# Optimization experiments

Hardware: AMD Instinct MI355X
Metric: run time of the kernel (lower is better)

The kernel has to match this reference:

```python
import jax, jax.numpy as jnp
import numpy as np

N_NODES = 50000
N_EDGES = 800000
HIDDEN = 128
MLP_DIM = 64

def setup_inputs() -> dict:
    key = jax.random.key(0)
    k1, k2, k3, k4 = jax.random.split(key, 4)
    node_emb = jax.random.normal(k1, (N_NODES, HIDDEN), dtype=jnp.float32)
    edge_index = jax.random.randint(k2, (2, N_EDGES), 0, N_NODES, dtype=jnp.int64)
    # Xavier-uniform init like the torch module
    lim1 = float(np.sqrt(6.0 / (2 * HIDDEN + MLP_DIM)))
    lim2 = float(np.sqrt(6.0 / (MLP_DIM + 1)))
    W1 = jax.random.uniform(k3, (2 * HIDDEN, MLP_DIM), minval=-lim1, maxval=lim1, dtype=jnp.float32)
    b1 = jnp.zeros((MLP_DIM,), dtype=jnp.float32)
    W2 = jax.random.uniform(k4, (MLP_DIM, 1), minval=-lim2, maxval=lim2, dtype=jnp.float32)
    b2 = jnp.zeros((1,), dtype=jnp.float32)
    return {"node_emb": node_emb, "edge_index": edge_index, "W1": W1, "b1": b1, "W2": W2, "b2": b2}

def reference(node_emb, edge_index, W1, b1, W2, b2):
    src, dst = edge_index[0], edge_index[1]
    emb_src = node_emb[src]                      # [E, H] gather
    emb_dst = node_emb[dst]                      # [E, H] gather
    edge_emb = jnp.concatenate([emb_src, emb_dst], axis=1)  # [E, 2H]
    h = jax.nn.relu(edge_emb @ W1 + b1)          # [E, MLP_DIM]
    edge_logits = h @ W2 + b2                    # [E, 1]
    return edge_logits
```

## Files before the change

kernel.cpp:

```cpp
#include <hip/hip_runtime.h>
#include <hip/hip_bf16.h>


#define HIDDEN 128

typedef __attribute__((ext_vector_type(8))) short bf16x8;
typedef __attribute__((ext_vector_type(4))) float f32x4;

__device__ inline unsigned short f32_to_bf16(float f) {
    unsigned int u = __float_as_uint(f);
    unsigned int r = (u + 0x7fffu + ((u >> 16) & 1u)) >> 16;
    return (unsigned short)r;
}

__global__ __launch_bounds__(256, 2) void precompute_pq_q8(
    const float* __restrict__ node_emb,
    const float* __restrict__ W1,
    const float* __restrict__ b1,
    unsigned char* __restrict__ P8,
    unsigned char* __restrict__ Q8,
    float* __restrict__ scl,
    int n_nodes)
{
    __shared__ unsigned short Bt[128 * 136];
    __shared__ unsigned char Out[64 * 144];

    const int t = threadIdx.x;
    const int wave = t >> 6, lane = t & 63;
    const int lrow = lane & 15;
    const int kq = (lane >> 4) * 8;
    const int m0 = blockIdx.x * 64;
    const int m = m0 + wave * 16 + lrow;
    const bool valid = (m < n_nodes);

    const float* arow = node_emb + (size_t)(valid ? m : 0) * HIDDEN + kq;
    float4 aLo[4], aHi[4];
    #pragma unroll
    for (int i = 0; i < 4; ++i) {
        if (valid) {
            aLo[i] = *(const float4*)(arow + i * 32);
            aHi[i] = *(const float4*)(arow + i * 32 + 4);
        } else {
            aLo[i] = make_float4(0.f, 0.f, 0.f, 0.f);
            aHi[i] = aLo[i];
        }
    }

    #pragma unroll
    for (int it = 0; it < 16; ++it) {
        int slot = it * 256 + t;
        int r = slot >> 4;
        int c4 = (slot & 15) * 4;
        float4 v = *(const float4*)&W1[r * 64 + c4];
        int j = (r < 128) ? c4 : (c4 + 64);
        int k = r & 127;
        Bt[(j + 0) * 136 + k] = f32_to_bf16(v.x);
        Bt[(j + 1) * 136 + k] = f32_to_bf16(v.y);
        Bt[(j + 2) * 136 + k] = f32_to_bf16(v.z);
        Bt[(j + 3) * 136 + k] = f32_to_bf16(v.w);
    }
    __syncthreads();

    f32x4 acc[8];
    #pragma unroll
    for (int c = 0; c < 8; ++c) acc[c] = (f32x4){0.f, 0.f, 0.f, 0.f};

    #pragma unroll
    for (int k0i = 0; k0i < 4; ++k0i) {
        union { bf16x8 v; __hip_bfloat162 h[4]; } ua;
        ua.h[0] = __float22bfloat162_rn(make_float2(aLo[k0i].x, aLo[k0i].y));
        ua.h[1] = __float22bfloat162_rn(make_float2(aLo[k0i].z, aLo[k0i].w));
        ua.h[2] = __float22bfloat162_rn(make_float2(aHi[k0i].x, aHi[k0i].y));
        ua.h[3] = __float22bfloat162_rn(make_float2(aHi[k0i].z, aHi[k0i].w));
        const int kbase = k0i * 32 + kq;
        #pragma unroll
        for (int c = 0; c < 8; ++c) {
            bf16x8 bf = *(const bf16x8*)&Bt[(c * 16 + lrow) * 136 + kbase];
            acc[c] = __builtin_amdgcn_mfma_f32_16x16x32_bf16(ua.v, bf, acc[c], 0, 0, 0);
        }
    }

    const int rbase = (lane >> 4) * 4;
    float sPv[4], sQv[4];
    #pragma unroll
    for (int reg = 0; reg < 4; ++reg) {
        const int row = wave * 16 + rbase + reg;
        float pv[4];
        #pragma unroll
        for (int c = 0; c < 4; ++c) pv[c] = acc[c][reg] + b1[c * 16 + lrow];
        float amaxP = fmaxf(fmaxf(fabsf(pv[0]), fabsf(pv[1])),
                            fmaxf(fabsf(pv[2]), fabsf(pv[3])));
        #pragma unroll
        for (int off = 1; off < 16; off <<= 1)
            amaxP = fmaxf(amaxP, __shfl_xor(amaxP, off, 64));
        float invP = (amaxP > 0.f) ? 127.f / amaxP : 0.f;
        sPv[reg] = amaxP * (1.f / 127.f);
        #pragma unroll
        for (int c = 0; c < 4; ++c)
            Out[row * 144 + c * 16 + lrow] =
                (unsigned char)((int)rintf(pv[c] * invP) + 128);
        float qv[4];
        #pragma unroll
        for (int c = 0; c < 4; ++c) qv[c] = acc[c + 4][reg];
        float amaxQ = fmaxf(fmaxf(fabsf(qv[0]), fabsf(qv[1])),
                            fmaxf(fabsf(qv[2]), fabsf(qv[3])));
        #pragma unroll
        for (int off = 1; off < 16; off <<= 1)
            amaxQ = fmaxf(amaxQ, __shfl_xor(amaxQ, off, 64));
        float invQ = (amaxQ > 0.f) ? 127.f / amaxQ : 0.f;
        sQv[reg] = amaxQ * (1.f / 127.f);
        #pragma unroll
        for (int c = 0; c < 4; ++c)
            Out[row * 144 + 64 + c * 16 + lrow] =
                (unsigned char)((int)rintf(qv[c] * invQ) + 128);
    }
    if (lrow == 0) {
        #pragma unroll
        for (int reg = 0; reg < 4; ++reg) {
            int mm = m0 + wave * 16 + rbase + reg;
            if (mm < n_nodes)
                *(float4*)&scl[(size_t)mm * 4] =
                    make_float4(sPv[reg], -128.f * sPv[reg],
                                sQv[reg], -128.f * sQv[reg]);
        }
    }
    __syncthreads();

    {
        int row = t >> 2, seg = (t & 3) * 16;
        int mm = m0 + row;
        if (mm < n_nodes) {
            *(int4*)&P8[(size_t)mm * 64 + seg] = *(const int4*)&Out[row * 144 + seg];
            *(int4*)&Q8[(size_t)mm * 64 + seg] = *(const int4*)&Out[row * 144 + 64 + seg];
        }
    }
}

__device__ inline float ub(unsigned int w, int b) {
    return (float)((w >> (b * 8)) & 0xffu);
}

__global__ __launch_bounds__(256) void edge_mlp_q8(
    const unsigned char* __restrict__ P8,
    const unsigned char* __restrict__ Q8,
    const float* __restrict__ scl,
    const int* __restrict__ edge_index,
    const float* __restrict__ W2,
    const float* __restrict__ b2,
    float* __restrict__ out,
    int E)
{
    const int t = threadIdx.x;
    const int g = t & 7;
    const int slot = t >> 3;
    const int e0 = blockIdx.x * 64 + slot;
    const int e1 = e0 + 32;

    float4 wA = *(const float4*)&W2[g * 8];
    float4 wB = *(const float4*)&W2[g * 8 + 4];

    const int src0 = edge_index[e0], dst0 = edge_index[E + e0];
    const int src1 = edge_index[e1], dst1 = edge_index[E + e1];

    uint2 p0 = *(const uint2*)&P8[(size_t)src0 * 64 + g * 8];
    uint2 q0 = *(const uint2*)&Q8[(size_t)dst0 * 64 + g * 8];
    uint2 p1 = *(const uint2*)&P8[(size_t)src1 * 64 + g * 8];
    uint2 q1 = *(const uint2*)&Q8[(size_t)dst1 * 64 + g * 8];

    float2 sp0 = *(const float2*)&scl[(size_t)src0 * 4];
    float2 sq0 = *(const float2*)&scl[(size_t)dst0 * 4 + 2];
    float2 sp1 = *(const float2*)&scl[(size_t)src1 * 4];
    float2 sq1 = *(const float2*)&scl[(size_t)dst1 * 4 + 2];

    const float o0 = sp0.y + sq0.y;
    const float o1 = sp1.y + sq1.y;

    float s0 = 0.f, s1 = 0.f;
    #pragma unroll
    for (int i = 0; i < 4; ++i) {
        float w = (i == 0) ? wA.x : (i == 1) ? wA.y : (i == 2) ? wA.z : wA.w;
        s0 += fmaxf(fmaf(ub(p0.x, i), sp0.x, fmaf(ub(q0.x, i), sq0.x, o0)), 0.f) * w;
        s1 += fmaxf(fmaf(ub(p1.x, i), sp1.x, fmaf(ub(q1.x, i), sq1.x, o1)), 0.f) * w;
    }
    #pragma unroll
    for (int i = 0; i < 4; ++i) {
        float w = (i == 0) ? wB.x : (i == 1) ? wB.y : (i == 2) ? wB.z : wB.w;
        s0 += fmaxf(fmaf(ub(p0.y, i), sp0.x, fmaf(ub(q0.y, i), sq0.x, o0)), 0.f) * w;
        s1 += fmaxf(fmaf(ub(p1.y, i), sp1.x, fmaf(ub(q1.y, i), sq1.x, o1)), 0.f) * w;
    }

    s0 += __shfl_xor(s0, 1, 64);  s1 += __shfl_xor(s1, 1, 64);
    s0 += __shfl_xor(s0, 2, 64);  s1 += __shfl_xor(s1, 2, 64);
    s0 += __shfl_xor(s0, 4, 64);  s1 += __shfl_xor(s1, 4, 64);

    if (g == 0) {
        float bb = b2[0];
        out[e0] = s0 + bb;
        out[e1] = s1 + bb;
    }
}

extern "C" void kernel_launch(void* const* d_in, const int* in_sizes, int n_in,
                              void* d_out, int out_size, void* d_ws, size_t ws_size,
                              hipStream_t stream) {
    const float* node_emb   = (const float*)d_in[0];
    const int*   edge_index = (const int*)d_in[1];
    const float* W1 = (const float*)d_in[2];
    const float* b1 = (const float*)d_in[3];
    const float* W2 = (const float*)d_in[4];
    const float* b2 = (const float*)d_in[5];
    float* out = (float*)d_out;

    const int n_nodes = in_sizes[0] / HIDDEN;
    const int E = in_sizes[1] / 2;

    unsigned char* P8 = (unsigned char*)d_ws;
    unsigned char* Q8 = P8 + (size_t)n_nodes * 64;
    float* scl = (float*)(Q8 + (size_t)n_nodes * 64);

    const int grid1 = (n_nodes + 63) / 64;
    precompute_pq_q8<<<grid1, 256, 0, stream>>>(node_emb, W1, b1, P8, Q8, scl, n_nodes);

    const int grid2 = (E + 63) / 64;
    edge_mlp_q8<<<grid2, 256, 0, stream>>>(P8, Q8, scl, edge_index, W2, b2, out, E);
}
```

Before: 116.9 us.

## Split edge MLP into two column-half passes over half-size gather tables

Splits the quantized P/Q tables into two 32-column halves and runs the edge kernel twice, each pass gathering only one half, so each pass's working set (about 1.6 MB per table) is more likely to stay cache-resident. Scales are stored as fp16 to shrink the scale table, and edge indices and outputs use nontemporal loads and stores. The cost is reading edge_index twice, plus a read-modify-write of the output in the second pass. The grid is now E/256 with no tail handling, which silently assumes E is a multiple of 256.

```diff
diff --git a/kernel.cpp b/kernel.cpp
--- a/kernel.cpp
+++ b/kernel.cpp
@@ -6,6 +6,7 @@
 
 typedef __attribute__((ext_vector_type(8))) short bf16x8;
 typedef __attribute__((ext_vector_type(4))) float f32x4;
+typedef __attribute__((ext_vector_type(4))) _Float16 half4f;
 
 __device__ inline unsigned short f32_to_bf16(float f) {
     unsigned int u = __float_as_uint(f);
@@ -17,9 +18,11 @@
     const float* __restrict__ node_emb,
     const float* __restrict__ W1,
     const float* __restrict__ b1,
-    unsigned char* __restrict__ P8,
-    unsigned char* __restrict__ Q8,
-    float* __restrict__ scl,
+    unsigned char* __restrict__ PA,
+    unsigned char* __restrict__ PB,
+    unsigned char* __restrict__ QA,
+    unsigned char* __restrict__ QB,
+    half4f* __restrict__ sclh,
     int n_nodes)
 {
     __shared__ unsigned short Bt[128 * 136];
@@ -99,6 +102,7 @@
         for (int c = 0; c < 4; ++c)
             Out[row * 144 + c * 16 + lrow] =
                 (unsigned char)((int)rintf(pv[c] * invP) + 128);
+
         float qv[4];
         #pragma unroll
         for (int c = 0; c < 4; ++c) qv[c] = acc[c + 4][reg];
@@ -118,20 +122,28 @@
         #pragma unroll
         for (int reg = 0; reg < 4; ++reg) {
             int mm = m0 + wave * 16 + rbase + reg;
-            if (mm < n_nodes)
-                *(float4*)&scl[(size_t)mm * 4] =
-                    make_float4(sPv[reg], -128.f * sPv[reg],
-                                sQv[reg], -128.f * sQv[reg]);
+            if (mm < n_nodes) {
+                half4f s;
+                s[0] = (_Float16)sPv[reg];
+                s[1] = (_Float16)(-128.f * sPv[reg]);
+                s[2] = (_Float16)sQv[reg];
+                s[3] = (_Float16)(-128.f * sQv[reg]);
+                sclh[mm] = s;
+            }
         }
     }
     __syncthreads();
 
     {
-        int row = t >> 2, seg = (t & 3) * 16;
+        int row = t & 63, quad = t >> 6;
         int mm = m0 + row;
         if (mm < n_nodes) {
-            *(int4*)&P8[(size_t)mm * 64 + seg] = *(const int4*)&Out[row * 144 + seg];
-            *(int4*)&Q8[(size_t)mm * 64 + seg] = *(const int4*)&Out[row * 144 + 64 + seg];
+            unsigned char* tab = (quad == 0) ? PA : (quad == 1) ? PB
+                               : (quad == 2) ? QA : QB;
+            const unsigned char* s = &Out[row * 144 + quad * 32];
+            unsigned char* d = tab + (size_t)mm * 32;
+            *(int4*)d = *(const int4*)s;
+            *(int4*)(d + 16) = *(const int4*)(s + 16);
         }
     }
 }
@@ -140,10 +152,30 @@
     return (float)((w >> (b * 8)) & 0xffu);
 }
 
-__global__ __launch_bounds__(256) void edge_mlp_q8(
-    const unsigned char* __restrict__ P8,
-    const unsigned char* __restrict__ Q8,
-    const float* __restrict__ scl,
+__device__ inline float edge_dot16(int4 p, int4 q, float sP, float sQ, float offs,
+                                   const float4& w0, const float4& w1,
+                                   const float4& w2v, const float4& w3) {
+    float s = 0.f;
+    const unsigned int pw[4] = {(unsigned)p.x, (unsigned)p.y, (unsigned)p.z, (unsigned)p.w};
+    const unsigned int qw[4] = {(unsigned)q.x, (unsigned)q.y, (unsigned)q.z, (unsigned)q.w};
+    const float4 wv[4] = {w0, w1, w2v, w3};
+    #pragma unroll
+    for (int d = 0; d < 4; ++d) {
+        const float* wf = (const float*)&wv[d];
+        #pragma unroll
+        for (int b = 0; b < 4; ++b) {
+            float x = fmaf(ub(pw[d], b), sP, fmaf(ub(qw[d], b), sQ, offs));
+            s = fmaf(fmaxf(x, 0.f), wf[b], s);
+        }
+    }
+    return s;
+}
+
+template <int HALF, bool ACCUM>
+__global__ __launch_bounds__(256) void edge_pass(
+    const unsigned char* __restrict__ Ptab,
+    const unsigned char* __restrict__ Qtab,
+    const half4f* __restrict__ sclh,
     const int* __restrict__ edge_index,
     const float* __restrict__ W2,
     const float* __restrict__ b2,
@@ -151,52 +183,51 @@
     int E)
 {
     const int t = threadIdx.x;
-    const int g = t & 7;
-    const int slot = t >> 3;
-    const int e0 = blockIdx.x * 64 + slot;
-    const int e1 = e0 + 32;
-
-    float4 wA = *(const float4*)&W2[g * 8];
-    float4 wB = *(const float4*)&W2[g * 8 + 4];
-
-    const int src0 = edge_index[e0], dst0 = edge_index[E + e0];
-    const int src1 = edge_index[e1], dst1 = edge_index[E + e1];
-
-    uint2 p0 = *(const uint2*)&P8[(size_t)src0 * 64 + g * 8];
-    uint2 q0 = *(const uint2*)&Q8[(size_t)dst0 * 64 + g * 8];
-    uint2 p1 = *(const uint2*)&P8[(size_t)src1 * 64 + g * 8];
-    uint2 q1 = *(const uint2*)&Q8[(size_t)dst1 * 64 + g * 8];
-
-    float2 sp0 = *(const float2*)&scl[(size_t)src0 * 4];
-    float2 sq0 = *(const float2*)&scl[(size_t)dst0 * 4 + 2];
-    float2 sp1 = *(const float2*)&scl[(size_t)src1 * 4];
-    float2 sq1 = *(const float2*)&scl[(size_t)dst1 * 4 + 2];
-
-    const float o0 = sp0.y + sq0.y;
-    const float o1 = sp1.y + sq1.y;
-
-    float s0 = 0.f, s1 = 0.f;
-    #pragma unroll
-    for (int i = 0; i < 4; ++i) {
-        float w = (i == 0) ? wA.x : (i == 1) ? wA.y : (i == 2) ? wA.z : wA.w;
-        s0 += fmaxf(fmaf(ub(p0.x, i), sp0.x, fmaf(ub(q0.x, i), sq0.x, o0)), 0.f) * w;
-        s1 += fmaxf(fmaf(ub(p1.x, i), sp1.x, fmaf(ub(q1.x, i), sq1.x, o1)), 0.f) * w;
-    }
-    #pragma unroll
-    for (int i = 0; i < 4; ++i) {
-        float w = (i == 0) ? wB.x : (i == 1) ? wB.y : (i == 2) ? wB.z : wB.w;
-        s0 += fmaxf(fmaf(ub(p0.y, i), sp0.x, fmaf(ub(q0.y, i), sq0.x, o0)), 0.f) * w;
-        s1 += fmaxf(fmaf(ub(p1.y, i), sp1.x, fmaf(ub(q1.y, i), sq1.x, o1)), 0.f) * w;
-    }
-
-    s0 += __shfl_xor(s0, 1, 64);  s1 += __shfl_xor(s1, 1, 64);
-    s0 += __shfl_xor(s0, 2, 64);  s1 += __shfl_xor(s1, 2, 64);
-    s0 += __shfl_xor(s0, 4, 64);  s1 += __shfl_xor(s1, 4, 64);
-
-    if (g == 0) {
-        float bb = b2[0];
-        out[e0] = s0 + bb;
-        out[e1] = s1 + bb;
+    const int h = t & 1;
+    const int slot = t >> 1;
+    const int e0 = blockIdx.x * 256 + slot;
+    const int e1 = e0 + 128;
+
+    const float* wbase = W2 + HALF * 32 + h * 16;
+    float4 w0 = *(const float4*)(wbase + 0);
+    float4 w1 = *(const float4*)(wbase + 4);
+    float4 w2v = *(const float4*)(wbase + 8);
+    float4 w3 = *(const float4*)(wbase + 12);
+
+    const int src0 = __builtin_nontemporal_load(&edge_index[e0]);
+    const int dst0 = __builtin_nontemporal_load(&edge_index[E + e0]);
+    const int src1 = __builtin_nontemporal_load(&edge_index[e1]);
+    const int dst1 = __builtin_nontemporal_load(&edge_index[E + e1]);
+
+    int4 p0 = *(const int4*)(Ptab + (size_t)src0 * 32 + h * 16);
+    int4 q0 = *(const int4*)(Qtab + (size_t)dst0 * 32 + h * 16);
+    int4 p1 = *(const int4*)(Ptab + (size_t)src1 * 32 + h * 16);
+    int4 q1 = *(const int4*)(Qtab + (size_t)dst1 * 32 + h * 16);
+
+    half4f sS0 = sclh[src0], sD0 = sclh[dst0];
+    half4f sS1 = sclh[src1], sD1 = sclh[dst1];
+    const float sP0 = (float)sS0[0], sQ0 = (float)sD0[2];
+    const float sP1 = (float)sS1[0], sQ1 = (float)sD1[2];
+    const float o0 = (float)sS0[1] + (float)sD0[3];
+    const float o1 = (float)sS1[1] + (float)sD1[3];
+
+    float s0 = edge_dot16(p0, q0, sP0, sQ0, o0, w0, w1, w2v, w3);
+    float s1 = edge_dot16(p1, q1, sP1, sQ1, o1, w0, w1, w2v, w3);
+
+    s0 += __shfl_xor(s0, 1, 64);
+    s1 += __shfl_xor(s1, 1, 64);
+
+    if (h == 0) {
+        if (ACCUM) {
+            float a0 = __builtin_nontemporal_load(&out[e0]);
+            float a1 = __builtin_nontemporal_load(&out[e1]);
+            __builtin_nontemporal_store(a0 + s0, &out[e0]);
+            __builtin_nontemporal_store(a1 + s1, &out[e1]);
+        } else {
+            float bb = b2[0];
+            __builtin_nontemporal_store(s0 + bb, &out[e0]);
+            __builtin_nontemporal_store(s1 + bb, &out[e1]);
+        }
     }
 }
 
@@ -214,13 +245,19 @@
     const int n_nodes = in_sizes[0] / HIDDEN;
     const int E = in_sizes[1] / 2;
 
-    unsigned char* P8 = (unsigned char*)d_ws;
-    unsigned char* Q8 = P8 + (size_t)n_nodes * 64;
-    float* scl = (float*)(Q8 + (size_t)n_nodes * 64);
+    unsigned char* PA = (unsigned char*)d_ws;
+    unsigned char* PB = PA + (size_t)n_nodes * 32;
+    unsigned char* QA = PB + (size_t)n_nodes * 32;
+    unsigned char* QB = QA + (size_t)n_nodes * 32;
+    half4f* sclh = (half4f*)(QB + (size_t)n_nodes * 32);
 
     const int grid1 = (n_nodes + 63) / 64;
-    precompute_pq_q8<<<grid1, 256, 0, stream>>>(node_emb, W1, b1, P8, Q8, scl, n_nodes);
-
-    const int grid2 = (E + 63) / 64;
-    edge_mlp_q8<<<grid2, 256, 0, stream>>>(P8, Q8, scl, edge_index, W2, b2, out, E);
-}
+    precompute_pq_q8<<<grid1, 256, 0, stream>>>(node_emb, W1, b1,
+                                                PA, PB, QA, QB, sclh, n_nodes);
+
+    const int grid2 = E / 256;
+    edge_pass<0, false><<<grid2, 256, 0, stream>>>(PA, QA, sclh, edge_index,
+                                                   W2, b2, out, E);
+    edge_pass<1, true><<<grid2, 256, 0, stream>>>(PB, QB, sclh, edge_index,
+                                                  W2, b2, out, E);
+}
```

Result: slower. 134.1 us (+14.8%).

## Pack 7-bit quantized P/Q tables with inline scale into 64-byte rows

Applied to the files above, without the earlier changes.

Quantizes the per-node P and Q projections to 7 bits instead of 8 and bit-packs 64 values plus the float scale into one 64-byte row per table. The separate scale array and its extra gathers go away, so each edge endpoint now needs a single cache line. The edge kernel is restructured to two threads per edge with wide loads, nontemporal loads and stores for edge indices and output, and a higher occupancy hint. In exchange there is more unpacking ALU work per element and coarser quantization that may hurt accuracy. The grid is now E/128 with no tail handling, which drops edges if E is not a multiple of 128.

```diff
diff --git a/kernel.cpp b/kernel.cpp
--- a/kernel.cpp
+++ b/kernel.cpp
@@ -3,9 +3,9 @@
 
 
 #define HIDDEN 128
-
 typedef __attribute__((ext_vector_type(8))) short bf16x8;
 typedef __attribute__((ext_vector_type(4))) float f32x4;
+typedef unsigned long long u64;
 
 __device__ inline unsigned short f32_to_bf16(float f) {
     unsigned int u = __float_as_uint(f);
@@ -13,17 +13,17 @@
     return (unsigned short)r;
 }
 
-__global__ __launch_bounds__(256, 2) void precompute_pq_q8(
+__global__ __launch_bounds__(256, 2) void precompute_pq_q7(
     const float* __restrict__ node_emb,
     const float* __restrict__ W1,
     const float* __restrict__ b1,
-    unsigned char* __restrict__ P8,
-    unsigned char* __restrict__ Q8,
-    float* __restrict__ scl,
+    unsigned char* __restrict__ Ptab,
+    unsigned char* __restrict__ Qtab,
     int n_nodes)
 {
     __shared__ unsigned short Bt[128 * 136];
     __shared__ unsigned char Out[64 * 144];
+    __shared__ float sArr[64][2];
 
     const int t = threadIdx.x;
     const int wave = t >> 6, lane = t & 63;
@@ -81,7 +81,6 @@
     }
 
     const int rbase = (lane >> 4) * 4;
-    float sPv[4], sQv[4];
     #pragma unroll
     for (int reg = 0; reg < 4; ++reg) {
         const int row = wave * 16 + rbase + reg;
@@ -93,12 +92,12 @@
         #pragma unroll
         for (int off = 1; off < 16; off <<= 1)
             amaxP = fmaxf(amaxP, __shfl_xor(amaxP, off, 64));
-        float invP = (amaxP > 0.f) ? 127.f / amaxP : 0.f;
-        sPv[reg] = amaxP * (1.f / 127.f);
+        float invP = (amaxP > 0.f) ? 63.f / amaxP : 0.f;
         #pragma unroll
         for (int c = 0; c < 4; ++c)
             Out[row * 144 + c * 16 + lrow] =
-                (unsigned char)((int)rintf(pv[c] * invP) + 128);
+                (unsigned char)((int)rintf(pv[c] * invP) + 64);
+
         float qv[4];
         #pragma unroll
         for (int c = 0; c < 4; ++c) qv[c] = acc[c + 4][reg];
@@ -107,43 +106,51 @@
         #pragma unroll
         for (int off = 1; off < 16; off <<= 1)
             amaxQ = fmaxf(amaxQ, __shfl_xor(amaxQ, off, 64));
-        float invQ = (amaxQ > 0.f) ? 127.f / amaxQ : 0.f;
-        sQv[reg] = amaxQ * (1.f / 127.f);
+        float invQ = (amaxQ > 0.f) ? 63.f / amaxQ : 0.f;
         #pragma unroll
         for (int c = 0; c < 4; ++c)
             Out[row * 144 + 64 + c * 16 + lrow] =
-                (unsigned char)((int)rintf(qv[c] * invQ) + 128);
-    }
-    if (lrow == 0) {
-        #pragma unroll
-        for (int reg = 0; reg < 4; ++reg) {
-            int mm = m0 + wave * 16 + rbase + reg;
-            if (mm < n_nodes)
-                *(float4*)&scl[(size_t)mm * 4] =
-                    make_float4(sPv[reg], -128.f * sPv[reg],
-                                sQv[reg], -128.f * sQv[reg]);
+                (unsigned char)((int)rintf(qv[c] * invQ) + 64);
+
+        if (lrow == 0) {
+            sArr[row][0] = (amaxP > 0.f) ? amaxP * (1.f / 63.f) : 0.f;
+            sArr[row][1] = (amaxQ > 0.f) ? amaxQ * (1.f / 63.f) : 0.f;
         }
     }
     __syncthreads();
 
     {
-        int row = t >> 2, seg = (t & 3) * 16;
-        int mm = m0 + row;
+        const int chunk = t & 1, tab = (t >> 1) & 1, row = t >> 2;
+        const int mm = m0 + row;
         if (mm < n_nodes) {
-            *(int4*)&P8[(size_t)mm * 64 + seg] = *(const int4*)&Out[row * 144 + seg];
-            *(int4*)&Q8[(size_t)mm * 64 + seg] = *(const int4*)&Out[row * 144 + 64 + seg];
-        }
-    }
-}
-
-__device__ inline float ub(unsigned int w, int b) {
-    return (float)((w >> (b * 8)) & 0xffu);
-}
-
-__global__ __launch_bounds__(256) void edge_mlp_q8(
-    const unsigned char* __restrict__ P8,
-    const unsigned char* __restrict__ Q8,
-    const float* __restrict__ scl,
+            const unsigned char* src = &Out[row * 144 + tab * 64 + chunk * 32];
+            u64 G[4];
+            #pragma unroll
+            for (int g = 0; g < 4; ++g) {
+                u64 B = *(const u64*)(src + g * 8);
+                u64 acc7 = 0;
+                #pragma unroll
+                for (int j = 0; j < 8; ++j)
+                    acc7 |= ((B >> (8 * j)) & 0x7fULL) << (7 * j);
+                G[g] = acc7;
+            }
+            float s = sArr[row][tab];
+            u64 R0 = G[0] | (G[1] << 56);
+            u64 R1 = (G[1] >> 8) | (G[2] << 48);
+            u64 R2 = (G[2] >> 16) | (G[3] << 40);
+            u64 R3 = (G[3] >> 24) | ((u64)__float_as_uint(s) << 32);
+            unsigned char* dst = ((tab == 0) ? Ptab : Qtab) + (size_t)mm * 64 + chunk * 32;
+            ((u64*)dst)[0] = R0;
+            ((u64*)dst)[1] = R1;
+            ((u64*)dst)[2] = R2;
+            ((u64*)dst)[3] = R3;
+        }
+    }
+}
+
+__global__ __launch_bounds__(256, 4) void edge_mlp_q7(
+    const unsigned char* __restrict__ Ptab,
+    const unsigned char* __restrict__ Qtab,
     const int* __restrict__ edge_index,
     const float* __restrict__ W2,
     const float* __restrict__ b2,
@@ -151,53 +158,59 @@
     int E)
 {
     const int t = threadIdx.x;
-    const int g = t & 7;
-    const int slot = t >> 3;
-    const int e0 = blockIdx.x * 64 + slot;
-    const int e1 = e0 + 32;
-
-    float4 wA = *(const float4*)&W2[g * 8];
-    float4 wB = *(const float4*)&W2[g * 8 + 4];
-
-    const int src0 = edge_index[e0], dst0 = edge_index[E + e0];
-    const int src1 = edge_index[e1], dst1 = edge_index[E + e1];
-
-    uint2 p0 = *(const uint2*)&P8[(size_t)src0 * 64 + g * 8];
-    uint2 q0 = *(const uint2*)&Q8[(size_t)dst0 * 64 + g * 8];
-    uint2 p1 = *(const uint2*)&P8[(size_t)src1 * 64 + g * 8];
-    uint2 q1 = *(const uint2*)&Q8[(size_t)dst1 * 64 + g * 8];
-
-    float2 sp0 = *(const float2*)&scl[(size_t)src0 * 4];
-    float2 sq0 = *(const float2*)&scl[(size_t)dst0 * 4 + 2];
-    float2 sp1 = *(const float2*)&scl[(size_t)src1 * 4];
-    float2 sq1 = *(const float2*)&scl[(size_t)dst1 * 4 + 2];
-
-    const float o0 = sp0.y + sq0.y;
-    const float o1 = sp1.y + sq1.y;
-
-    float s0 = 0.f, s1 = 0.f;
-    #pragma unroll
-    for (int i = 0; i < 4; ++i) {
-        float w = (i == 0) ? wA.x : (i == 1) ? wA.y : (i == 2) ? wA.z : wA.w;
-        s0 += fmaxf(fmaf(ub(p0.x, i), sp0.x, fmaf(ub(q0.x, i), sq0.x, o0)), 0.f) * w;
-        s1 += fmaxf(fmaf(ub(p1.x, i), sp1.x, fmaf(ub(q1.x, i), sq1.x, o1)), 0.f) * w;
-    }
-    #pragma unroll
-    for (int i = 0; i < 4; ++i) {
-        float w = (i == 0) ? wB.x : (i == 1) ? wB.y : (i == 2) ? wB.z : wB.w;
-        s0 += fmaxf(fmaf(ub(p0.y, i), sp0.x, fmaf(ub(q0.y, i), sq0.x, o0)), 0.f) * w;
-        s1 += fmaxf(fmaf(ub(p1.y, i), sp1.x, fmaf(ub(q1.y, i), sq1.x, o1)), 0.f) * w;
-    }
-
-    s0 += __shfl_xor(s0, 1, 64);  s1 += __shfl_xor(s1, 1, 64);
-    s0 += __shfl_xor(s0, 2, 64);  s1 += __shfl_xor(s1, 2, 64);
-    s0 += __shfl_xor(s0, 4, 64);  s1 += __shfl_xor(s1, 4, 64);
-
-    if (g == 0) {
-        float bb = b2[0];
-        out[e0] = s0 + bb;
-        out[e1] = s1 + bb;
-    }
+    const int h = t & 1;
+    const int e = blockIdx.x * 128 + (t >> 1);
+
+    const int src = __builtin_nontemporal_load(&edge_index[e]);
+    const int dst = __builtin_nontemporal_load(&edge_index[E + e]);
+
+    const unsigned char* pc = Ptab + (size_t)src * 64 + h * 32;
+    const unsigned char* qc = Qtab + (size_t)dst * 64 + h * 32;
+    uint4 pA = *(const uint4*)pc;
+    uint4 pB = *(const uint4*)(pc + 16);
+    uint4 qA = *(const uint4*)qc;
+    uint4 qB = *(const uint4*)(qc + 16);
+
+    const float* wp = W2 + h * 32;
+    float4 wv[8];
+    #pragma unroll
+    for (int k = 0; k < 8; ++k) wv[k] = *(const float4*)(wp + 4 * k);
+
+    u64 PR0 = pA.x | ((u64)pA.y << 32), PR1 = pA.z | ((u64)pA.w << 32);
+    u64 PR2 = pB.x | ((u64)pB.y << 32), PR3 = pB.z | ((u64)pB.w << 32);
+    u64 QR0 = qA.x | ((u64)qA.y << 32), QR1 = qA.z | ((u64)qA.w << 32);
+    u64 QR2 = qB.x | ((u64)qB.y << 32), QR3 = qB.z | ((u64)qB.w << 32);
+
+    u64 PG[4], QG[4];
+    PG[0] = PR0 & 0x00ffffffffffffffULL;
+    PG[1] = (PR0 >> 56) | ((PR1 & 0x0000ffffffffffffULL) << 8);
+    PG[2] = (PR1 >> 48) | ((PR2 & 0x000000ffffffffffULL) << 16);
+    PG[3] = (PR2 >> 40) | ((PR3 & 0x00000000ffffffffULL) << 24);
+    QG[0] = QR0 & 0x00ffffffffffffffULL;
+    QG[1] = (QR0 >> 56) | ((QR1 & 0x0000ffffffffffffULL) << 8);
+    QG[2] = (QR1 >> 48) | ((QR2 & 0x000000ffffffffffULL) << 16);
+    QG[3] = (QR2 >> 40) | ((QR3 & 0x00000000ffffffffULL) << 24);
+
+    const float sP = __uint_as_float((unsigned int)(PR3 >> 32));
+    const float sQ = __uint_as_float((unsigned int)(QR3 >> 32));
+    const float offs = -64.f * (sP + sQ);
+
+    float s = 0.f;
+    #pragma unroll
+    for (int g = 0; g < 4; ++g) {
+        const float* wf = (const float*)&wv[2 * g];
+        #pragma unroll
+        for (int j = 0; j < 8; ++j) {
+            float fp = (float)((unsigned int)(PG[g] >> (7 * j)) & 127u);
+            float fq = (float)((unsigned int)(QG[g] >> (7 * j)) & 127u);
+            float x = fmaf(fp, sP, fmaf(fq, sQ, offs));
+            s = fmaf(fmaxf(x, 0.f), wf[j], s);
+        }
+    }
+
+    s += __shfl_xor(s, 1, 64);
+    if (h == 0)
+        __builtin_nontemporal_store(s + b2[0], &out[e]);
 }
 
 extern "C" void kernel_launch(void* const* d_in, const int* in_sizes, int n_in,
@@ -214,13 +227,15 @@
     const int n_nodes = in_sizes[0] / HIDDEN;
     const int E = in_sizes[1] / 2;
 
-    unsigned char* P8 = (unsigned char*)d_ws;
-    unsigned char* Q8 = P8 + (size_t)n_nodes * 64;
-    float* scl = (float*)(Q8 + (size_t)n_nodes * 64);
+    const int n_pad = ((n_nodes + 63) / 64) * 64;
+    unsigned char* Ptab = (unsigned char*)d_ws;
+    unsigned char* Qtab = Ptab + (size_t)n_pad * 64;
 
     const int grid1 = (n_nodes + 63) / 64;
-    precompute_pq_q8<<<grid1, 256, 0, stream>>>(node_emb, W1, b1, P8, Q8, scl, n_nodes);
-
-    const int grid2 = (E + 63) / 64;
-    edge_mlp_q8<<<grid2, 256, 0, stream>>>(P8, Q8, scl, edge_index, W2, b2, out, E);
-}
+    precompute_pq_q7<<<grid1, 256, 0, stream>>>(node_emb, W1, b1,
+                                                Ptab, Qtab, n_nodes);
+
+    const int grid2 = E / 128;
+    edge_mlp_q7<<<grid2, 256, 0, stream>>>(Ptab, Qtab, edge_index,
+                                           W2, b2, out, E);
+}
```

Result: no change. 115.1 us (-1.5%).
